# Kernel optimization log

Measured on AMD Instinct MI355X. Metric: run time of the kernel, lower is better.

Reference implementation:

```python
import jax, jax.numpy as jnp
import numpy as np

N_GRAPHS = 8


def glorot(key, shape):
    fan_in, fan_out = shape[0], shape[1]
    s = (6.0 / (fan_in + fan_out)) ** 0.5
    return jax.random.uniform(key, shape, jnp.float32, -s, s)


def setup_inputs() -> dict:
    key = jax.random.key(0)
    ks = jax.random.split(key, 8)
    N, E, C = 100000, 800000, 128
    x = jax.random.normal(ks[0], (N, C), jnp.float32)
    edge_index = jax.random.randint(ks[1], (2, E), 0, N, jnp.int64)
    batch = jnp.sort(jax.random.randint(ks[2], (N,), 0, N_GRAPHS, jnp.int64))
    W1 = glorot(ks[3], (C, 64));   b1 = jnp.zeros((64,), jnp.float32)
    W2 = glorot(ks[4], (64, 128)); b2 = jnp.zeros((128,), jnp.float32)
    W3 = glorot(ks[5], (128, 256)); b3 = jnp.zeros((256,), jnp.float32)
    Wfc = glorot(ks[6], (256, 1))
    bfc = jax.random.normal(ks[7], (1,), jnp.float32) * 0.01
    return {"x": x, "edge_index": edge_index, "batch": batch,
            "W1": W1, "b1": b1, "W2": W2, "b2": b2, "W3": W3, "b3": b3,
            "Wfc": Wfc, "bfc": bfc}


def _gcn_layer(h_in, W, b, src, dst, norm_edge, self_coef, n):
    # GCNConv: x' = D^{-1/2}(A+I)D^{-1/2} (x W) + b   (self-loops included)
    h = h_in @ W                                     # [N, out]
    msg = h[src] * norm_edge[:, None]                # gather + edge normalize
    agg = jax.ops.segment_sum(msg, dst, num_segments=n)  # scatter-add
    agg = agg + h * self_coef[:, None]               # self-loop contribution
    return agg + b


def reference(x, edge_index, batch, W1, b1, W2, b2, W3, b3, Wfc, bfc):
    n = x.shape[0]
    src, dst = edge_index[0], edge_index[1]
    # gcn_norm with self-loops: deg = in-degree + 1
    deg = jax.ops.segment_sum(jnp.ones_like(dst, dtype=x.dtype), dst, num_segments=n) + 1.0
    dis = deg ** -0.5
    norm_edge = dis[src] * dis[dst]
    self_coef = dis * dis
    h = jax.nn.relu(_gcn_layer(x, W1, b1, src, dst, norm_edge, self_coef, n))
    h = jax.nn.relu(_gcn_layer(h, W2, b2, src, dst, norm_edge, self_coef, n))
    h = jax.nn.relu(_gcn_layer(h, W3, b3, src, dst, norm_edge, self_coef, n))
    # global_mean_pool over graphs
    counts = jax.ops.segment_sum(jnp.ones((n,), x.dtype), batch, num_segments=N_GRAPHS)
    pooled = jax.ops.segment_sum(h, batch, num_segments=N_GRAPHS) / counts[:, None]
    return pooled @ Wfc + bfc
```

## Files before the change

kernel.cpp:

```cpp
#include <hip/hip_runtime.h>
#include <hip/hip_bf16.h>

typedef __attribute__((ext_vector_type(8))) short short8v;
typedef __attribute__((ext_vector_type(4))) float f32x4;

static __device__ __forceinline__ unsigned short f2bf(float f) {
  __hip_bfloat16 b = __float2bfloat16(f);
  return *reinterpret_cast<unsigned short*>(&b);
}
static __device__ __forceinline__ float bf2f(unsigned short u) {
  unsigned int x = ((unsigned int)u) << 16;
  return __builtin_bit_cast(float, x);
}
static __device__ __forceinline__ float bflo(unsigned int u) {
  return __builtin_bit_cast(float, u << 16);
}
static __device__ __forceinline__ float bfhi(unsigned int u) {
  return __builtin_bit_cast(float, u & 0xffff0000u);
}

__global__ __launch_bounds__(256) void k_hist(const int* __restrict__ ei,
                                              int* __restrict__ cnt, int E) {
  int stride = gridDim.x * blockDim.x;
  for (int i = blockIdx.x * blockDim.x + threadIdx.x; i < E; i += stride)
    atomicAdd(&cnt[ei[E + i]], 1);
}

__global__ __launch_bounds__(256) void k_scan1(const int* __restrict__ cnt,
                                               int* __restrict__ row_tmp,
                                               int* __restrict__ bsum, int N) {
  __shared__ int sd[256];
  const int tid = threadIdx.x;
  const int i = blockIdx.x * 256 + tid;
  int v = (i < N) ? cnt[i] : 0;
  sd[tid] = v;
  __syncthreads();
#pragma unroll
  for (int off = 1; off < 256; off <<= 1) {
    int t = (tid >= off) ? sd[tid - off] : 0;
    __syncthreads();
    sd[tid] += t;
    __syncthreads();
  }
  if (i < N) row_tmp[i] = sd[tid] - v;
  if (tid == 255) bsum[blockIdx.x] = sd[255];
}

__global__ __launch_bounds__(1024) void k_scan2(int* __restrict__ bsum, int nb) {
  __shared__ int sd[1024];
  const int t = threadIdx.x;
  int v = (t < nb) ? bsum[t] : 0;
  sd[t] = v;
  __syncthreads();
#pragma unroll
  for (int off = 1; off < 1024; off <<= 1) {
    int x = (t >= off) ? sd[t - off] : 0;
    __syncthreads();
    sd[t] += x;
    __syncthreads();
  }
  if (t < nb) bsum[t] = sd[t] - v;
}

__global__ __launch_bounds__(256) void k_scan3(const int* __restrict__ row_tmp,
                                               const int* __restrict__ bsum,
                                               const int* __restrict__ cnt,
                                               const int* __restrict__ batch,
                                               float* __restrict__ dis,
                                               int* __restrict__ row_ptr,
                                               int* __restrict__ bucket_cur,
                                               int* __restrict__ gstart, int N,
                                               int E) {
  const int i = blockIdx.x * 256 + threadIdx.x;
  if (i < N) {
    int rp = row_tmp[i] + bsum[i >> 8];
    row_ptr[i] = rp;
    if ((i & 255) == 0) bucket_cur[i >> 8] = rp;
    dis[i] = 1.0f / sqrtf((float)cnt[i] + 1.0f);
    int b = batch[i];
    if (i == 0) {
      for (int g = 0; g <= b; ++g) gstart[g] = 0;
    } else {
      int p = batch[i - 1];
      for (int g = p + 1; g <= b; ++g) gstart[g] = i;
    }
    if (i == N - 1)
      for (int g = b + 1; g <= 8; ++g) gstart[g] = N;
  }
  if (i == 0) row_ptr[N] = E;
}

__global__ __launch_bounds__(256) void k_b3(const int* __restrict__ ei,
                                            int* __restrict__ bucket_cur,
                                            uint2* __restrict__ pairs, int E) {
  __shared__ int cntD[512];
  __shared__ int gbase[512];
  const int t = threadIdx.x;
  for (int i = t; i < 512; i += 256) cntD[i] = 0;
  __syncthreads();
  const int base = blockIdx.x * 2048;
  int s[8], d[8], rk[8];
#pragma unroll
  for (int i = 0; i < 8; ++i) {
    int e = base + i * 256 + t;
    if (e < E) {
      s[i] = ei[e];
      d[i] = ei[E + e];
      rk[i] = atomicAdd(&cntD[d[i] >> 8], 1);
    }
  }
  __syncthreads();
  for (int i = t; i < 512; i += 256)
    if (cntD[i] > 0) gbase[i] = atomicAdd(&bucket_cur[i], cntD[i]);
  __syncthreads();
#pragma unroll
  for (int i = 0; i < 8; ++i) {
    int e = base + i * 256 + t;
    if (e < E)
      pairs[gbase[d[i] >> 8] + rk[i]] = make_uint2((unsigned)s[i], (unsigned)d[i]);
  }
}

__global__ __launch_bounds__(256) void k_b4(const int* __restrict__ row_ptr,
                                            const uint2* __restrict__ pairs,
                                            int* __restrict__ col, int N) {
  __shared__ int curL[257];
  const int n0 = blockIdx.x << 8;
  const int nn = min(256, N - n0);
  const int t = threadIdx.x;
  for (int i = t; i <= nn; i += 256) curL[i] = row_ptr[n0 + i];
  __syncthreads();
  const int p0 = curL[0], p1 = curL[nn];
  __syncthreads();
  for (int idx = p0 + t; idx < p1; idx += 256) {
    uint2 pr = pairs[idx];
    int pos = atomicAdd(&curL[(int)pr.y - n0], 1);
    col[pos] = (int)pr.x;
  }
}

static __device__ __forceinline__ void pack_one(const float* __restrict__ W,
                                                unsigned short* __restrict__ Wp,
                                                int K, int M, int t) {
  int KT = K >> 5;
  int lane = t & 63;
  int tile = t >> 6;
  int kt = tile % KT;
  int ct = tile / KT;
  int c = ct * 16 + (lane & 15);
  int k0 = kt * 32 + (lane >> 4) * 8;
  unsigned short v[8];
#pragma unroll
  for (int j = 0; j < 8; ++j) v[j] = f2bf(W[(size_t)(k0 + j) * M + c]);
  ushort4* dst = (ushort4*)&Wp[(size_t)t * 8];
  dst[0] = make_ushort4(v[0], v[1], v[2], v[3]);
  dst[1] = make_ushort4(v[4], v[5], v[6], v[7]);
}

__global__ __launch_bounds__(256) void k_packall(
    const float* __restrict__ W1, const float* __restrict__ W2,
    const float* __restrict__ W3, unsigned short* __restrict__ Wp1,
    unsigned short* __restrict__ Wp2, unsigned short* __restrict__ Wp3) {
  int t = blockIdx.x * 256 + threadIdx.x;
  if (t < 1024)
    pack_one(W1, Wp1, 128, 64, t);
  else if (t < 2048)
    pack_one(W2, Wp2, 64, 128, t - 1024);
  else if (t < 6144)
    pack_one(W3, Wp3, 128, 256, t - 2048);
}

template <bool EPI>
__global__ __launch_bounds__(256) void k_agg64(const int* __restrict__ row_ptr,
                                               const int* __restrict__ col,
                                               const float* __restrict__ dis,
                                               const unsigned short* __restrict__ Hin,
                                               const float* __restrict__ bias,
                                               unsigned short* __restrict__ Pout,
                                               int N) {
  const int lane = threadIdx.x & 63;
  int d = blockIdx.x * 4 + (threadIdx.x >> 6);
  if (d >= N) return;
  const int q = lane >> 3;
  const int cl = lane & 7;
  const int cb = cl * 8;
  const float disd = dis[d];
  const int beg = row_ptr[d];
  const int end = row_ptr[d + 1];
  const int deg = end - beg;
  const int nedge = min(deg, 64);

  int s_l = d;
  float w_l = 0.f;
  if (lane < nedge) {
    s_l = col[beg + lane];
    w_l = dis[s_l] * disd;
  }

  float acc[8];
#pragma unroll
  for (int k = 0; k < 8; ++k) acc[k] = 0.f;
  if (q == 0) {
    uint4 u = *(const uint4*)&Hin[(size_t)d * 64 + cb];
    const float sc = disd * disd;
    acc[0] = bflo(u.x) * sc; acc[1] = bfhi(u.x) * sc;
    acc[2] = bflo(u.y) * sc; acc[3] = bfhi(u.y) * sc;
    acc[4] = bflo(u.z) * sc; acc[5] = bfhi(u.z) * sc;
    acc[6] = bflo(u.w) * sc; acc[7] = bfhi(u.w) * sc;
  }

  const int padded = (nedge + 15) & ~15;
  for (int base = 0; base < padded; base += 16) {
    int e0 = base + q, e1 = base + 8 + q;
    int s0 = __shfl(s_l, e0, 64);
    float w0 = __shfl(w_l, e0, 64);
    int s1 = __shfl(s_l, e1, 64);
    float w1 = __shfl(w_l, e1, 64);
    if (e0 >= nedge) { s0 = d; w0 = 0.f; }
    if (e1 >= nedge) { s1 = d; w1 = 0.f; }
    uint4 u0 = *(const uint4*)&Hin[(size_t)s0 * 64 + cb];
    uint4 u1 = *(const uint4*)&Hin[(size_t)s1 * 64 + cb];
    acc[0] = fmaf(bflo(u0.x), w0, acc[0]); acc[1] = fmaf(bfhi(u0.x), w0, acc[1]);
    acc[2] = fmaf(bflo(u0.y), w0, acc[2]); acc[3] = fmaf(bfhi(u0.y), w0, acc[3]);
    acc[4] = fmaf(bflo(u0.z), w0, acc[4]); acc[5] = fmaf(bfhi(u0.z), w0, acc[5]);
    acc[6] = fmaf(bflo(u0.w), w0, acc[6]); acc[7] = fmaf(bfhi(u0.w), w0, acc[7]);
    acc[0] = fmaf(bflo(u1.x), w1, acc[0]); acc[1] = fmaf(bfhi(u1.x), w1, acc[1]);
    acc[2] = fmaf(bflo(u1.y), w1, acc[2]); acc[3] = fmaf(bfhi(u1.y), w1, acc[3]);
    acc[4] = fmaf(bflo(u1.z), w1, acc[4]); acc[5] = fmaf(bfhi(u1.z), w1, acc[5]);
    acc[6] = fmaf(bflo(u1.w), w1, acc[6]); acc[7] = fmaf(bfhi(u1.w), w1, acc[7]);
  }
  if (deg > 64) {
    for (int j = beg + 64 + q; j < end; j += 8) {
      int s = col[j];
      float w = dis[s] * disd;
      uint4 u = *(const uint4*)&Hin[(size_t)s * 64 + cb];
      acc[0] = fmaf(bflo(u.x), w, acc[0]); acc[1] = fmaf(bfhi(u.x), w, acc[1]);
      acc[2] = fmaf(bflo(u.y), w, acc[2]); acc[3] = fmaf(bfhi(u.y), w, acc[3]);
      acc[4] = fmaf(bflo(u.z), w, acc[4]); acc[5] = fmaf(bfhi(u.z), w, acc[5]);
      acc[6] = fmaf(bflo(u.w), w, acc[6]); acc[7] = fmaf(bfhi(u.w), w, acc[7]);
    }
  }

#pragma unroll
  for (int k = 0; k < 8; ++k) {
    acc[k] += __shfl_xor(acc[k], 8, 64);
    acc[k] += __shfl_xor(acc[k], 16, 64);
    acc[k] += __shfl_xor(acc[k], 32, 64);
  }
  if (q == 0) {
    if (EPI) {
#pragma unroll
      for (int k = 0; k < 8; ++k) acc[k] = fmaxf(acc[k] + bias[cb + k], 0.f);
    }
    uint4 o;
    o.x = (unsigned)f2bf(acc[0]) | ((unsigned)f2bf(acc[1]) << 16);
    o.y = (unsigned)f2bf(acc[2]) | ((unsigned)f2bf(acc[3]) << 16);
    o.z = (unsigned)f2bf(acc[4]) | ((unsigned)f2bf(acc[5]) << 16);
    o.w = (unsigned)f2bf(acc[6]) | ((unsigned)f2bf(acc[7]) << 16);
    *(uint4*)&Pout[(size_t)d * 64 + cb] = o;
  }
}

__global__ __launch_bounds__(256) void k_agg128(const int* __restrict__ row_ptr,
                                                const int* __restrict__ col,
                                                const float* __restrict__ dis,
                                                const unsigned short* __restrict__ Hin,
                                                unsigned short* __restrict__ Pout,
                                                int N) {
  const int lane = threadIdx.x & 63;
  int d = blockIdx.x * 4 + (threadIdx.x >> 6);
  if (d >= N) return;
  const int q = lane >> 4;
  const int cl = lane & 15;
  const int cb = cl * 8;
  const float disd = dis[d];
  const int beg = row_ptr[d];
  const int end = row_ptr[d + 1];
  const int deg = end - beg;
  const int nedge = min(deg, 64);

  int s_l = d;
  float w_l = 0.f;
  if (lane < nedge) {
    s_l = col[beg + lane];
    w_l = dis[s_l] * disd;
  }

  float acc[8];
#pragma unroll
  for (int k = 0; k < 8; ++k) acc[k] = 0.f;
  if (q == 0) {
    uint4 u = *(const uint4*)&Hin[(size_t)d * 128 + cb];
    const float sc = disd * disd;
    acc[0] = bflo(u.x) * sc; acc[1] = bfhi(u.x) * sc;
    acc[2] = bflo(u.y) * sc; acc[3] = bfhi(u.y) * sc;
    acc[4] = bflo(u.z) * sc; acc[5] = bfhi(u.z) * sc;
    acc[6] = bflo(u.w) * sc; acc[7] = bfhi(u.w) * sc;
  }

  const int padded = (nedge + 7) & ~7;
  for (int base = 0; base < padded; base += 8) {
    int e0 = base + q, e1 = base + 4 + q;
    int s0 = __shfl(s_l, e0, 64);
    float w0 = __shfl(w_l, e0, 64);
    int s1 = __shfl(s_l, e1, 64);
    float w1 = __shfl(w_l, e1, 64);
    if (e0 >= nedge) { s0 = d; w0 = 0.f; }
    if (e1 >= nedge) { s1 = d; w1 = 0.f; }
    uint4 u0 = *(const uint4*)&Hin[(size_t)s0 * 128 + cb];
    uint4 u1 = *(const uint4*)&Hin[(size_t)s1 * 128 + cb];
    acc[0] = fmaf(bflo(u0.x), w0, acc[0]); acc[1] = fmaf(bfhi(u0.x), w0, acc[1]);
    acc[2] = fmaf(bflo(u0.y), w0, acc[2]); acc[3] = fmaf(bfhi(u0.y), w0, acc[3]);
    acc[4] = fmaf(bflo(u0.z), w0, acc[4]); acc[5] = fmaf(bfhi(u0.z), w0, acc[5]);
    acc[6] = fmaf(bflo(u0.w), w0, acc[6]); acc[7] = fmaf(bfhi(u0.w), w0, acc[7]);
    acc[0] = fmaf(bflo(u1.x), w1, acc[0]); acc[1] = fmaf(bfhi(u1.x), w1, acc[1]);
    acc[2] = fmaf(bflo(u1.y), w1, acc[2]); acc[3] = fmaf(bfhi(u1.y), w1, acc[3]);
    acc[4] = fmaf(bflo(u1.z), w1, acc[4]); acc[5] = fmaf(bfhi(u1.z), w1, acc[5]);
    acc[6] = fmaf(bflo(u1.w), w1, acc[6]); acc[7] = fmaf(bfhi(u1.w), w1, acc[7]);
  }
  if (deg > 64) {
    for (int j = beg + 64 + q; j < end; j += 4) {
      int s = col[j];
      float w = dis[s] * disd;
      uint4 u = *(const uint4*)&Hin[(size_t)s * 128 + cb];
      acc[0] = fmaf(bflo(u.x), w, acc[0]); acc[1] = fmaf(bfhi(u.x), w, acc[1]);
      acc[2] = fmaf(bflo(u.y), w, acc[2]); acc[3] = fmaf(bfhi(u.y), w, acc[3]);
      acc[4] = fmaf(bflo(u.z), w, acc[4]); acc[5] = fmaf(bfhi(u.z), w, acc[5]);
      acc[6] = fmaf(bflo(u.w), w, acc[6]); acc[7] = fmaf(bfhi(u.w), w, acc[7]);
    }
  }

#pragma unroll
  for (int k = 0; k < 8; ++k) {
    acc[k] += __shfl_xor(acc[k], 16, 64);
    acc[k] += __shfl_xor(acc[k], 32, 64);
  }
  if (q == 0) {
    uint4 o;
    o.x = (unsigned)f2bf(acc[0]) | ((unsigned)f2bf(acc[1]) << 16);
    o.y = (unsigned)f2bf(acc[2]) | ((unsigned)f2bf(acc[3]) << 16);
    o.z = (unsigned)f2bf(acc[4]) | ((unsigned)f2bf(acc[5]) << 16);
    o.w = (unsigned)f2bf(acc[6]) | ((unsigned)f2bf(acc[7]) << 16);
    *(uint4*)&Pout[(size_t)d * 128 + cb] = o;
  }
}

template <int K, int M, bool F32IN, bool BIAS>
__global__ __launch_bounds__(256) void k_mm(const void* __restrict__ Ap,
                                            const unsigned short* __restrict__ Wp,
                                            const float* __restrict__ bias,
                                            unsigned short* __restrict__ Hout,
                                            int N) {
  constexpr int KT = K / 32, CT = M / 16;
  const int lane = threadIdx.x & 63;
  const int wid = threadIdx.x >> 6;
  int row0 = (blockIdx.x * 4 + wid) * 16;
  row0 = __builtin_amdgcn_readfirstlane(row0);
  if (row0 >= N) return;
  const int r = lane & 15;
  const int kh = lane >> 4;

  int arow = row0 + r;
  if (arow >= N) arow = N - 1;

  f32x4 acc[CT];
#pragma unroll
  for (int ct = 0; ct < CT; ++ct) acc[ct] = (f32x4){0.f, 0.f, 0.f, 0.f};

#pragma unroll
  for (int kt = 0; kt < KT; ++kt) {
    short8v a;
    if (F32IN) {
      const float* Af = (const float*)Ap;
      const float* p = &Af[(size_t)arow * K + kt * 32 + kh * 8];
      float4 f0 = *(const float4*)p;
      float4 f1 = *(const float4*)(p + 4);
      a[0] = (short)f2bf(f0.x); a[1] = (short)f2bf(f0.y);
      a[2] = (short)f2bf(f0.z); a[3] = (short)f2bf(f0.w);
      a[4] = (short)f2bf(f1.x); a[5] = (short)f2bf(f1.y);
      a[6] = (short)f2bf(f1.z); a[7] = (short)f2bf(f1.w);
    } else {
      const unsigned short* Ab = (const unsigned short*)Ap;
      a = *(const short8v*)&Ab[(size_t)arow * K + kt * 32 + kh * 8];
    }
#pragma unroll
    for (int ct = 0; ct < CT; ++ct) {
      short8v b = *(const short8v*)&Wp[(size_t)((ct * KT + kt) * 64 + lane) * 8];
      acc[ct] = __builtin_amdgcn_mfma_f32_16x16x32_bf16(a, b, acc[ct], 0, 0, 0);
    }
  }

  const int orow0 = row0 + kh * 4;
#pragma unroll
  for (int ct = 0; ct < CT; ++ct) {
    const int c = ct * 16 + r;
    const float bv = BIAS ? bias[c] : 0.f;
#pragma unroll
    for (int reg = 0; reg < 4; ++reg) {
      int row = orow0 + reg;
      if (row < N) {
        float v = acc[ct][reg] + bv;
        if (BIAS) v = fmaxf(v, 0.f);
        Hout[(size_t)row * M + c] = f2bf(v);
      }
    }
  }
}

__global__ __launch_bounds__(256) void k_pool2(const unsigned short* __restrict__ H4,
                                               const int* __restrict__ gstart,
                                               float* __restrict__ pooled) {
  __shared__ float sd[8][256];
  const int g = blockIdx.y;
  const int s = gstart[g], e = gstart[g + 1];
  if (s >= e) return;
  const int PB = gridDim.x;
  const int chunk = (e - s + PB - 1) / PB;
  const int r0 = s + blockIdx.x * chunk;
  const int r1 = min(e, r0 + chunk);

  const int t = threadIdx.x;
  const int rs = t >> 5;
  const int cl = t & 31;
  const int cb = cl * 8;

  float a[8];
#pragma unroll
  for (int k = 0; k < 8; ++k) a[k] = 0.f;

  for (int r = r0 + rs; r < r1; r += 8) {
    uint4 u = *(const uint4*)&H4[(size_t)r * 256 + cb];
    a[0] += bflo(u.x); a[1] += bfhi(u.x);
    a[2] += bflo(u.y); a[3] += bfhi(u.y);
    a[4] += bflo(u.z); a[5] += bfhi(u.z);
    a[6] += bflo(u.w); a[7] += bfhi(u.w);
  }
#pragma unroll
  for (int k = 0; k < 8; ++k) sd[rs][cb + k] = a[k];
  __syncthreads();
  float v = 0.f;
#pragma unroll
  for (int q = 0; q < 8; ++q) v += sd[q][t];
  atomicAdd(&pooled[g * 256 + t], v);
}

__global__ __launch_bounds__(256) void k_final(const float* __restrict__ pooled,
                                               const int* __restrict__ gstart,
                                               const float* __restrict__ Wfc,
                                               const float* __restrict__ bfc,
                                               float* __restrict__ out) {
  __shared__ float red[4];
  const int t = threadIdx.x;
  for (int g = 0; g < 8; ++g) {
    float cg = (float)(gstart[g + 1] - gstart[g]);
    float v = pooled[g * 256 + t] / cg * Wfc[t];
#pragma unroll
    for (int off = 32; off > 0; off >>= 1) v += __shfl_down(v, off, 64);
    if ((t & 63) == 0) red[t >> 6] = v;
    __syncthreads();
    if (t == 0) out[g] = red[0] + red[1] + red[2] + red[3] + bfc[0];
    __syncthreads();
  }
}

extern "C" void kernel_launch(void* const* d_in, const int* in_sizes, int n_in,
                              void* d_out, int out_size, void* d_ws,
                              size_t ws_size, hipStream_t stream) {
  const float* x = (const float*)d_in[0];
  const int* ei = (const int*)d_in[1];
  const int* batch = (const int*)d_in[2];
  const float* W1 = (const float*)d_in[3];
  const float* b1 = (const float*)d_in[4];
  const float* W2 = (const float*)d_in[5];
  const float* b2 = (const float*)d_in[6];
  const float* W3 = (const float*)d_in[7];
  const float* b3 = (const float*)d_in[8];
  const float* Wfc = (const float*)d_in[9];
  const float* bfc = (const float*)d_in[10];
  float* out = (float*)d_out;

  const int N = in_sizes[0] / 128;
  const int E = in_sizes[1] / 2;
  const int nb = (N + 255) / 256;
  const int nbk = (N + 255) >> 8;

  float* ws = (float*)d_ws;
  size_t o = 0;
  float* dis = ws + o;            o += (size_t)N;
  int* cnt = (int*)(ws + o);      o += (size_t)N;
  int* row_tmp = (int*)(ws + o);  o += (size_t)N;
  int* bsum = (int*)(ws + o);     o += 1024;
  int* row_ptr = (int*)(ws + o);  o += (size_t)N + 1;
  int* bucket_cur = (int*)(ws + o); o += 512;
  int* col = (int*)(ws + o);      o += (size_t)E;
  uint2* pairs = (uint2*)(ws + o); o += (size_t)E * 2;
  float* pooled = ws + o;         o += 2048;
  int* gstart = (int*)(ws + o);   o += 16;
  unsigned short* Wp1 = (unsigned short*)(ws + o); o += 4096;
  unsigned short* Wp2 = (unsigned short*)(ws + o); o += 4096;
  unsigned short* Wp3 = (unsigned short*)(ws + o); o += 16384;
  o = (o + 63) & ~(size_t)63;
  unsigned short* bufA = (unsigned short*)(ws + o); o += (size_t)N * 32;
  unsigned short* bufB = (unsigned short*)(ws + o); o += (size_t)N * 32;
  unsigned short* bufC = (unsigned short*)(ws + o); o += (size_t)N * 64;
  unsigned short* bufD = (unsigned short*)(ws + o); o += (size_t)N * 64;
  unsigned short* bufE = (unsigned short*)(ws + o); o += (size_t)N * 128;

  hipMemsetAsync(cnt, 0, (size_t)N * sizeof(int), stream);
  hipMemsetAsync(pooled, 0, 2048 * sizeof(float), stream);

  k_hist<<<2048, 256, 0, stream>>>(ei, cnt, E);
  k_scan1<<<nb, 256, 0, stream>>>(cnt, row_tmp, bsum, N);
  k_scan2<<<1, 1024, 0, stream>>>(bsum, nb);
  k_scan3<<<nb, 256, 0, stream>>>(row_tmp, bsum, cnt, batch, dis, row_ptr,
                                  bucket_cur, gstart, N, E);
  k_b3<<<(E + 2047) / 2048, 256, 0, stream>>>(ei, bucket_cur, pairs, E);
  k_b4<<<nbk, 256, 0, stream>>>(row_ptr, pairs, col, N);
  k_packall<<<24, 256, 0, stream>>>(W1, W2, W3, Wp1, Wp2, Wp3);

  const int ablocks = (N + 3) / 4;
  const int mblocks = (N + 63) / 64;
  k_mm<128, 64, true, false><<<mblocks, 256, 0, stream>>>(x, Wp1, nullptr, bufA, N);
  k_agg64<true><<<ablocks, 256, 0, stream>>>(row_ptr, col, dis, bufA, b1, bufB, N);
  k_agg64<false><<<ablocks, 256, 0, stream>>>(row_ptr, col, dis, bufB, nullptr, bufA, N);
  k_mm<64, 128, false, true><<<mblocks, 256, 0, stream>>>(bufA, Wp2, b2, bufC, N);
  k_agg128<<<ablocks, 256, 0, stream>>>(row_ptr, col, dis, bufC, bufD, N);
  k_mm<128, 256, false, true><<<mblocks, 256, 0, stream>>>(bufD, Wp3, b3, bufE, N);

  k_pool2<<<dim3(128, 8), 256, 0, stream>>>(bufE, gstart, pooled);
  k_final<<<1, 256, 0, stream>>>(pooled, gstart, Wfc, bfc, out);
}
```

Baseline: 391.2 us.

## Fuse final GEMM with mean pooling and stage k_mm output through LDS

The last GCN layer's matmul now accumulates its ReLU outputs directly into per-graph pooled sums using partitioned atomics, instead of writing a 256-wide hidden buffer and reading it back in a separate pool kernel. A wave whose rows all belong to one graph reduces with shuffles before issuing the atomic. k_final sums the 32 partitions. Separately, k_mm writes its tile into LDS and then stores it with coalesced 16-byte writes. The cost is atomic traffic and an extra LDS round trip plus a barrier.

```diff
diff --git a/kernel.cpp b/kernel.cpp
--- a/kernel.cpp
+++ b/kernel.cpp
@@ -3,6 +3,8 @@
 
 typedef __attribute__((ext_vector_type(8))) short short8v;
 typedef __attribute__((ext_vector_type(4))) float f32x4;
+
+#define PART 32
 
 static __device__ __forceinline__ unsigned short f2bf(float f) {
   __hip_bfloat16 b = __float2bfloat16(f);
@@ -352,6 +354,83 @@
                                             unsigned short* __restrict__ Hout,
                                             int N) {
   constexpr int KT = K / 32, CT = M / 16;
+  __shared__ unsigned short lds[64][M + 8];
+  const int lane = threadIdx.x & 63;
+  const int wid = threadIdx.x >> 6;
+  const int blk0 = blockIdx.x * 64;
+  int row0 = blk0 + wid * 16;
+  row0 = __builtin_amdgcn_readfirstlane(row0);
+  const bool active = row0 < N;
+  const int r = lane & 15;
+  const int kh = lane >> 4;
+
+  if (active) {
+    int arow = row0 + r;
+    if (arow >= N) arow = N - 1;
+
+    f32x4 acc[CT];
+#pragma unroll
+    for (int ct = 0; ct < CT; ++ct) acc[ct] = (f32x4){0.f, 0.f, 0.f, 0.f};
+
+#pragma unroll
+    for (int kt = 0; kt < KT; ++kt) {
+      short8v a;
+      if (F32IN) {
+        const float* Af = (const float*)Ap;
+        const float* p = &Af[(size_t)arow * K + kt * 32 + kh * 8];
+        float4 f0 = *(const float4*)p;
+        float4 f1 = *(const float4*)(p + 4);
+        a[0] = (short)f2bf(f0.x); a[1] = (short)f2bf(f0.y);
+        a[2] = (short)f2bf(f0.z); a[3] = (short)f2bf(f0.w);
+        a[4] = (short)f2bf(f1.x); a[5] = (short)f2bf(f1.y);
+        a[6] = (short)f2bf(f1.z); a[7] = (short)f2bf(f1.w);
+      } else {
+        const unsigned short* Ab = (const unsigned short*)Ap;
+        a = *(const short8v*)&Ab[(size_t)arow * K + kt * 32 + kh * 8];
+      }
+#pragma unroll
+      for (int ct = 0; ct < CT; ++ct) {
+        short8v b = *(const short8v*)&Wp[(size_t)((ct * KT + kt) * 64 + lane) * 8];
+        acc[ct] = __builtin_amdgcn_mfma_f32_16x16x32_bf16(a, b, acc[ct], 0, 0, 0);
+      }
+    }
+
+    const int lrow0 = wid * 16 + kh * 4;
+#pragma unroll
+    for (int ct = 0; ct < CT; ++ct) {
+      const int c = ct * 16 + r;
+      const float bv = BIAS ? bias[c] : 0.f;
+#pragma unroll
+      for (int reg = 0; reg < 4; ++reg) {
+        float v = acc[ct][reg] + bv;
+        if (BIAS) v = fmaxf(v, 0.f);
+        lds[lrow0 + reg][c] = f2bf(v);
+      }
+    }
+  }
+  __syncthreads();
+  constexpr int CBK = M / 8;
+  constexpr int ITER = 64 * CBK / 256;
+  const int t = threadIdx.x;
+#pragma unroll
+  for (int it = 0; it < ITER; ++it) {
+    int idx = it * 256 + t;
+    int row = idx / CBK;
+    int cbk = idx % CBK;
+    if (blk0 + row < N)
+      *(uint4*)&Hout[(size_t)(blk0 + row) * M + cbk * 8] =
+          *(const uint4*)&lds[row][cbk * 8];
+  }
+}
+
+template <int K, int M>
+__global__ __launch_bounds__(256) void k_mmpool(const unsigned short* __restrict__ Ab,
+                                                const unsigned short* __restrict__ Wp,
+                                                const float* __restrict__ bias,
+                                                const int* __restrict__ batch,
+                                                float* __restrict__ pooled_part,
+                                                int N) {
+  constexpr int KT = K / 32, CT = M / 16;
   const int lane = threadIdx.x & 63;
   const int wid = threadIdx.x >> 6;
   int row0 = (blockIdx.x * 4 + wid) * 16;
@@ -369,20 +448,7 @@
 
 #pragma unroll
   for (int kt = 0; kt < KT; ++kt) {
-    short8v a;
-    if (F32IN) {
-      const float* Af = (const float*)Ap;
-      const float* p = &Af[(size_t)arow * K + kt * 32 + kh * 8];
-      float4 f0 = *(const float4*)p;
-      float4 f1 = *(const float4*)(p + 4);
-      a[0] = (short)f2bf(f0.x); a[1] = (short)f2bf(f0.y);
-      a[2] = (short)f2bf(f0.z); a[3] = (short)f2bf(f0.w);
-      a[4] = (short)f2bf(f1.x); a[5] = (short)f2bf(f1.y);
-      a[6] = (short)f2bf(f1.z); a[7] = (short)f2bf(f1.w);
-    } else {
-      const unsigned short* Ab = (const unsigned short*)Ap;
-      a = *(const short8v*)&Ab[(size_t)arow * K + kt * 32 + kh * 8];
-    }
+    short8v a = *(const short8v*)&Ab[(size_t)arow * K + kt * 32 + kh * 8];
 #pragma unroll
     for (int ct = 0; ct < CT; ++ct) {
       short8v b = *(const short8v*)&Wp[(size_t)((ct * KT + kt) * 64 + lane) * 8];
@@ -391,60 +457,36 @@
   }
 
   const int orow0 = row0 + kh * 4;
+  const int rlast = min(row0 + 15, N - 1);
+  const int g0 = batch[row0];
+  const bool uni = (batch[rlast] == g0);
+  float* pp = pooled_part + (size_t)(blockIdx.x & (PART - 1)) * 2048;
+
 #pragma unroll
   for (int ct = 0; ct < CT; ++ct) {
     const int c = ct * 16 + r;
-    const float bv = BIAS ? bias[c] : 0.f;
+    const float bv = bias[c];
+    float s = 0.f;
 #pragma unroll
     for (int reg = 0; reg < 4; ++reg) {
       int row = orow0 + reg;
-      if (row < N) {
-        float v = acc[ct][reg] + bv;
-        if (BIAS) v = fmaxf(v, 0.f);
-        Hout[(size_t)row * M + c] = f2bf(v);
+      float v = fmaxf(acc[ct][reg] + bv, 0.f);
+      if (row >= N) v = 0.f;
+      if (uni) {
+        s += v;
+      } else if (row < N) {
+        atomicAdd(&pp[batch[row] * 256 + c], v);
       }
     }
-  }
-}
-
-__global__ __launch_bounds__(256) void k_pool2(const unsigned short* __restrict__ H4,
-                                               const int* __restrict__ gstart,
-                                               float* __restrict__ pooled) {
-  __shared__ float sd[8][256];
-  const int g = blockIdx.y;
-  const int s = gstart[g], e = gstart[g + 1];
-  if (s >= e) return;
-  const int PB = gridDim.x;
-  const int chunk = (e - s + PB - 1) / PB;
-  const int r0 = s + blockIdx.x * chunk;
-  const int r1 = min(e, r0 + chunk);
-
-  const int t = threadIdx.x;
-  const int rs = t >> 5;
-  const int cl = t & 31;
-  const int cb = cl * 8;
-
-  float a[8];
-#pragma unroll
-  for (int k = 0; k < 8; ++k) a[k] = 0.f;
-
-  for (int r = r0 + rs; r < r1; r += 8) {
-    uint4 u = *(const uint4*)&H4[(size_t)r * 256 + cb];
-    a[0] += bflo(u.x); a[1] += bfhi(u.x);
-    a[2] += bflo(u.y); a[3] += bfhi(u.y);
-    a[4] += bflo(u.z); a[5] += bfhi(u.z);
-    a[6] += bflo(u.w); a[7] += bfhi(u.w);
-  }
-#pragma unroll
-  for (int k = 0; k < 8; ++k) sd[rs][cb + k] = a[k];
-  __syncthreads();
-  float v = 0.f;
-#pragma unroll
-  for (int q = 0; q < 8; ++q) v += sd[q][t];
-  atomicAdd(&pooled[g * 256 + t], v);
-}
-
-__global__ __launch_bounds__(256) void k_final(const float* __restrict__ pooled,
+    if (uni) {
+      s += __shfl_xor(s, 16, 64);
+      s += __shfl_xor(s, 32, 64);
+      if (lane < 16) atomicAdd(&pp[g0 * 256 + c], s);
+    }
+  }
+}
+
+__global__ __launch_bounds__(256) void k_final(const float* __restrict__ pooled_part,
                                                const int* __restrict__ gstart,
                                                const float* __restrict__ Wfc,
                                                const float* __restrict__ bfc,
@@ -452,8 +494,10 @@
   __shared__ float red[4];
   const int t = threadIdx.x;
   for (int g = 0; g < 8; ++g) {
+    float v = 0.f;
+    for (int p = 0; p < PART; ++p) v += pooled_part[p * 2048 + g * 256 + t];
     float cg = (float)(gstart[g + 1] - gstart[g]);
-    float v = pooled[g * 256 + t] / cg * Wfc[t];
+    v = v / cg * Wfc[t];
 #pragma unroll
     for (int off = 32; off > 0; off >>= 1) v += __shfl_down(v, off, 64);
     if ((t & 63) == 0) red[t >> 6] = v;
@@ -494,7 +538,7 @@
   int* bucket_cur = (int*)(ws + o); o += 512;
   int* col = (int*)(ws + o);      o += (size_t)E;
   uint2* pairs = (uint2*)(ws + o); o += (size_t)E * 2;
-  float* pooled = ws + o;         o += 2048;
+  float* pooled_part = ws + o;    o += (size_t)PART * 2048;
   int* gstart = (int*)(ws + o);   o += 16;
   unsigned short* Wp1 = (unsigned short*)(ws + o); o += 4096;
   unsigned short* Wp2 = (unsigned short*)(ws + o); o += 4096;
@@ -504,10 +548,9 @@
   unsigned short* bufB = (unsigned short*)(ws + o); o += (size_t)N * 32;
   unsigned short* bufC = (unsigned short*)(ws + o); o += (size_t)N * 64;
   unsigned short* bufD = (unsigned short*)(ws + o); o += (size_t)N * 64;
-  unsigned short* bufE = (unsigned short*)(ws + o); o += (size_t)N * 128;
 
   hipMemsetAsync(cnt, 0, (size_t)N * sizeof(int), stream);
-  hipMemsetAsync(pooled, 0, 2048 * sizeof(float), stream);
+  hipMemsetAsync(pooled_part, 0, (size_t)PART * 2048 * sizeof(float), stream);
 
   k_hist<<<2048, 256, 0, stream>>>(ei, cnt, E);
   k_scan1<<<nb, 256, 0, stream>>>(cnt, row_tmp, bsum, N);
@@ -525,8 +568,8 @@
   k_agg64<false><<<ablocks, 256, 0, stream>>>(row_ptr, col, dis, bufB, nullptr, bufA, N);
   k_mm<64, 128, false, true><<<mblocks, 256, 0, stream>>>(bufA, Wp2, b2, bufC, N);
   k_agg128<<<ablocks, 256, 0, stream>>>(row_ptr, col, dis, bufC, bufD, N);
-  k_mm<128, 256, false, true><<<mblocks, 256, 0, stream>>>(bufD, Wp3, b3, bufE, N);
-
-  k_pool2<<<dim3(128, 8), 256, 0, stream>>>(bufE, gstart, pooled);
-  k_final<<<1, 256, 0, stream>>>(pooled, gstart, Wfc, bfc, out);
-}
+  k_mmpool<128, 256><<<(N + 63) / 64, 256, 0, stream>>>(bufD, Wp3, b3, batch,
+                                                        pooled_part, N);
+
+  k_final<<<1, 256, 0, stream>>>(pooled_part, gstart, Wfc, bfc, out);
+}
```

New measurement: 406.3 us. 3.9% more time.

## Split GEMM output columns across waves and stage outputs through LDS for coalesced stores

Applied to the files above, without the earlier changes.

The dense transform kernel now has each wave own a column slice for all 64 rows of the block, instead of each wave computing every column for its own 16 rows. Each wave loads the A rows for all four row tiles and reuses each B fragment across four MFMAs, so per-wave weight traffic drops. Results are written to shared memory and then copied out as 16-byte coalesced rows, replacing scattered 2-byte global stores. This costs more register pressure, one block barrier, and redundant A loads across waves, which should mostly hit in cache.

```diff
diff --git a/kernel.cpp b/kernel.cpp
--- a/kernel.cpp
+++ b/kernel.cpp
@@ -346,64 +346,85 @@
 }
 
 template <int K, int M, bool F32IN, bool BIAS>
-__global__ __launch_bounds__(256) void k_mm(const void* __restrict__ Ap,
-                                            const unsigned short* __restrict__ Wp,
-                                            const float* __restrict__ bias,
-                                            unsigned short* __restrict__ Hout,
-                                            int N) {
-  constexpr int KT = K / 32, CT = M / 16;
+__global__ __launch_bounds__(256) void k_mmx(const void* __restrict__ Ap,
+                                             const unsigned short* __restrict__ Wp,
+                                             const float* __restrict__ bias,
+                                             unsigned short* __restrict__ Hout,
+                                             int N) {
+  constexpr int KT = K / 32, CTW = M / 64;
+  __shared__ unsigned short lds[64][M + 8];
   const int lane = threadIdx.x & 63;
   const int wid = threadIdx.x >> 6;
-  int row0 = (blockIdx.x * 4 + wid) * 16;
-  row0 = __builtin_amdgcn_readfirstlane(row0);
-  if (row0 >= N) return;
+  const int blk0 = blockIdx.x * 64;
   const int r = lane & 15;
   const int kh = lane >> 4;
 
-  int arow = row0 + r;
-  if (arow >= N) arow = N - 1;
-
-  f32x4 acc[CT];
-#pragma unroll
-  for (int ct = 0; ct < CT; ++ct) acc[ct] = (f32x4){0.f, 0.f, 0.f, 0.f};
+  int ar[4];
+#pragma unroll
+  for (int rt = 0; rt < 4; ++rt) ar[rt] = min(blk0 + rt * 16 + r, N - 1);
+
+  f32x4 acc[4][CTW];
+#pragma unroll
+  for (int rt = 0; rt < 4; ++rt)
+#pragma unroll
+    for (int c = 0; c < CTW; ++c) acc[rt][c] = (f32x4){0.f, 0.f, 0.f, 0.f};
 
 #pragma unroll
   for (int kt = 0; kt < KT; ++kt) {
-    short8v a;
-    if (F32IN) {
-      const float* Af = (const float*)Ap;
-      const float* p = &Af[(size_t)arow * K + kt * 32 + kh * 8];
-      float4 f0 = *(const float4*)p;
-      float4 f1 = *(const float4*)(p + 4);
-      a[0] = (short)f2bf(f0.x); a[1] = (short)f2bf(f0.y);
-      a[2] = (short)f2bf(f0.z); a[3] = (short)f2bf(f0.w);
-      a[4] = (short)f2bf(f1.x); a[5] = (short)f2bf(f1.y);
-      a[6] = (short)f2bf(f1.z); a[7] = (short)f2bf(f1.w);
-    } else {
-      const unsigned short* Ab = (const unsigned short*)Ap;
-      a = *(const short8v*)&Ab[(size_t)arow * K + kt * 32 + kh * 8];
-    }
-#pragma unroll
-    for (int ct = 0; ct < CT; ++ct) {
+    short8v a[4];
+#pragma unroll
+    for (int rt = 0; rt < 4; ++rt) {
+      if (F32IN) {
+        const float* Af = (const float*)Ap;
+        const float* p = &Af[(size_t)ar[rt] * K + kt * 32 + kh * 8];
+        float4 f0 = *(const float4*)p;
+        float4 f1 = *(const float4*)(p + 4);
+        a[rt][0] = (short)f2bf(f0.x); a[rt][1] = (short)f2bf(f0.y);
+        a[rt][2] = (short)f2bf(f0.z); a[rt][3] = (short)f2bf(f0.w);
+        a[rt][4] = (short)f2bf(f1.x); a[rt][5] = (short)f2bf(f1.y);
+        a[rt][6] = (short)f2bf(f1.z); a[rt][7] = (short)f2bf(f1.w);
+      } else {
+        const unsigned short* Ab = (const unsigned short*)Ap;
+        a[rt] = *(const short8v*)&Ab[(size_t)ar[rt] * K + kt * 32 + kh * 8];
+      }
+    }
+#pragma unroll
+    for (int c = 0; c < CTW; ++c) {
+      const int ct = wid * CTW + c;
       short8v b = *(const short8v*)&Wp[(size_t)((ct * KT + kt) * 64 + lane) * 8];
-      acc[ct] = __builtin_amdgcn_mfma_f32_16x16x32_bf16(a, b, acc[ct], 0, 0, 0);
-    }
-  }
-
-  const int orow0 = row0 + kh * 4;
-#pragma unroll
-  for (int ct = 0; ct < CT; ++ct) {
-    const int c = ct * 16 + r;
-    const float bv = BIAS ? bias[c] : 0.f;
-#pragma unroll
-    for (int reg = 0; reg < 4; ++reg) {
-      int row = orow0 + reg;
-      if (row < N) {
-        float v = acc[ct][reg] + bv;
+#pragma unroll
+      for (int rt = 0; rt < 4; ++rt)
+        acc[rt][c] = __builtin_amdgcn_mfma_f32_16x16x32_bf16(a[rt], b, acc[rt][c], 0, 0, 0);
+    }
+  }
+
+#pragma unroll
+  for (int c = 0; c < CTW; ++c) {
+    const int col = (wid * CTW + c) * 16 + r;
+    const float bv = BIAS ? bias[col] : 0.f;
+#pragma unroll
+    for (int rt = 0; rt < 4; ++rt) {
+      const int lrow0 = rt * 16 + kh * 4;
+#pragma unroll
+      for (int reg = 0; reg < 4; ++reg) {
+        float v = acc[rt][c][reg] + bv;
         if (BIAS) v = fmaxf(v, 0.f);
-        Hout[(size_t)row * M + c] = f2bf(v);
+        lds[lrow0 + reg][col] = f2bf(v);
       }
     }
+  }
+  __syncthreads();
+  constexpr int CBK = M / 8;
+  constexpr int ITER = 64 * CBK / 256;
+  const int t = threadIdx.x;
+#pragma unroll
+  for (int it = 0; it < ITER; ++it) {
+    int idx = it * 256 + t;
+    int row = idx / CBK;
+    int cbk = idx % CBK;
+    if (blk0 + row < N)
+      *(uint4*)&Hout[(size_t)(blk0 + row) * M + cbk * 8] =
+          *(const uint4*)&lds[row][cbk * 8];
   }
 }
 
@@ -520,12 +541,12 @@
 
   const int ablocks = (N + 3) / 4;
   const int mblocks = (N + 63) / 64;
-  k_mm<128, 64, true, false><<<mblocks, 256, 0, stream>>>(x, Wp1, nullptr, bufA, N);
+  k_mmx<128, 64, true, false><<<mblocks, 256, 0, stream>>>(x, Wp1, nullptr, bufA, N);
   k_agg64<true><<<ablocks, 256, 0, stream>>>(row_ptr, col, dis, bufA, b1, bufB, N);
   k_agg64<false><<<ablocks, 256, 0, stream>>>(row_ptr, col, dis, bufB, nullptr, bufA, N);
-  k_mm<64, 128, false, true><<<mblocks, 256, 0, stream>>>(bufA, Wp2, b2, bufC, N);
+  k_mmx<64, 128, false, true><<<mblocks, 256, 0, stream>>>(bufA, Wp2, b2, bufC, N);
   k_agg128<<<ablocks, 256, 0, stream>>>(row_ptr, col, dis, bufC, bufD, N);
-  k_mm<128, 256, false, true><<<mblocks, 256, 0, stream>>>(bufD, Wp3, b3, bufE, N);
+  k_mmx<128, 256, false, true><<<mblocks, 256, 0, stream>>>(bufD, Wp3, b3, bufE, N);
 
   k_pool2<<<dim3(128, 8), 256, 0, stream>>>(bufE, gstart, pooled);
   k_final<<<1, 256, 0, stream>>>(pooled, gstart, Wfc, bfc, out);
```

Result: no change. 385.5 us (-1.4%).
